# Optimization experiments

Measured on AMD Instinct MI355X. Metric: run time of the kernel, lower is better.

The kernel has to match this reference:

```python
import jax, jax.numpy as jnp
import numpy as np

B, L, D = 16, 2048, 128
NEG = -1000000.0  # fill value used by the torch module

def setup_inputs() -> dict:
    key = jax.random.key(0)
    kq, kk, kv, kl = jax.random.split(key, 4)
    Q = jax.random.normal(kq, (B, L, D), dtype=jnp.float32)
    K = jax.random.normal(kk, (B, L, D), dtype=jnp.float32)
    V = jax.random.normal(kv, (B, L, D), dtype=jnp.float32)
    valid_lens = jax.random.randint(kl, (B,), 0, L, dtype=jnp.int32)
    return {"Q": Q, "K": K, "V": V, "valid_lens": valid_lens}

def reference(Q, K, V, valid_lens):
    d = Q.shape[-1]
    scale = 1.0 / jnp.sqrt(jnp.asarray(d, Q.dtype))
    # scores: [B, Lq, Lk]
    scores = jnp.einsum("bqd,bkd->bqk", Q, K) * scale
    # mask[b, q, k] = k < valid_lens[b]  (torch code requires Lq == Lk)
    mask = jnp.arange(scores.shape[-1])[None, None, :] < valid_lens[:, None, None]
    scores = jnp.where(mask, scores, jnp.asarray(NEG, scores.dtype))
    weights = jax.nn.softmax(scores, axis=-1)
    # dropout=0.0 / eval mode -> identity
    return jnp.einsum("bqk,bkd->bqd", weights, V)
```

## Files before the change

kernel.cpp:

```cpp
#include <hip/hip_runtime.h>
#include <hip/hip_bf16.h>
#include <math.h>

#define NB 16
#define NL 2048
#define ND 128
#define QT 64
#define KT 32
#define NTILE (NL / KT)
#define NEGV -1000000.0f
#define SCL 0.08838834764831845f

typedef short bfrag __attribute__((ext_vector_type(8)));
typedef float f32x4 __attribute__((ext_vector_type(4)));
typedef short s16x4 __attribute__((ext_vector_type(4)));
typedef short s16x8 __attribute__((ext_vector_type(8)));

typedef const __attribute__((address_space(1))) void* gas_ptr;
typedef __attribute__((address_space(3))) void* las_ptr;

__device__ __forceinline__ short f2bf(float f) {
    unsigned u = __float_as_uint(f);
    unsigned r = u + 0x7FFFu + ((u >> 16) & 1u);
    return (short)(r >> 16);
}
__device__ __forceinline__ float bf2f(short h) {
    return __uint_as_float(((unsigned)(unsigned short)h) << 16);
}

__device__ __forceinline__ int kswz(int r, int c) { return (r * ND + c) ^ ((r & 7) << 3); }
__device__ __forceinline__ int vswz(int d, int k) { return (d * KT + k) ^ (((d >> 1) & 3) << 3); }
__device__ __forceinline__ int pswz(int q, int k) { return (q * KT + k) ^ (((q >> 1) & 3) << 3); }

__global__ __launch_bounds__(512) void prep_k(const float* __restrict__ Kg,
                                              short* __restrict__ KWS) {
    const int bt = blockIdx.x;
    const int g = threadIdx.x;
    const int r = g >> 4, ccd = g & 15;
    const int ccs = ccd ^ (r & 7);
    const float* src = Kg + ((size_t)((bt >> 6) * NL) + (bt & 63) * KT + r) * ND + ccs * 8;
    f32x4 a0 = *(const f32x4*)src;
    f32x4 a1 = *(const f32x4*)(src + 4);
    float vals[8] = {a0[0], a0[1], a0[2], a0[3], a1[0], a1[1], a1[2], a1[3]};
    s16x8 h, l;
    #pragma unroll
    for (int j = 0; j < 8; ++j) {
        short hb = f2bf(vals[j]);
        h[j] = hb;
        l[j] = f2bf(vals[j] - bf2f(hb));
    }
    short* dst = KWS + (size_t)bt * 2 * 4096 + g * 8;
    *(s16x8*)dst = h;
    *(s16x8*)(dst + 4096) = l;
}

__global__ __launch_bounds__(512) void prep_v(const float* __restrict__ Vg,
                                              short* __restrict__ VWS) {
    const int bt = blockIdx.x;
    const int g = threadIdx.x;
    const int ch = g >> 7, d = g & 127;
    const int chs = ch ^ ((d >> 1) & 3);
    const float* src = Vg + ((size_t)((bt >> 6) * NL) + (bt & 63) * KT + chs * 8) * ND + d;
    s16x8 h, l;
    #pragma unroll
    for (int j = 0; j < 8; ++j) {
        float f = src[(size_t)j * ND];
        short hb = f2bf(f);
        h[j] = hb;
        l[j] = f2bf(f - bf2f(hb));
    }
    short* dst = VWS + (size_t)bt * 2 * 4096 + (d * 4 + ch) * 8;
    *(s16x8*)dst = h;
    *(s16x8*)(dst + 4096) = l;
}

__global__ __launch_bounds__(256, 2) void attn_fwd(
    const float* __restrict__ Qg, const int* __restrict__ vlens,
    const short* __restrict__ KWS, const short* __restrict__ VWS,
    float* __restrict__ Og)
{
    __shared__ __align__(16) short kv[2][4][4096];
    __shared__ __align__(16) short ph[4][512], pl[4][512];

    const int tid = threadIdx.x;
    const int wv = tid >> 6, lane = tid & 63;
    const int lq = lane & 15, lg = lane >> 4;

    const int bid = blockIdx.x;
    const int xcd = bid & 7, slot = bid >> 3;
    const int b = xcd * 2 + (slot >> 5);
    const int qblk = slot & 31;
    const int q0 = qblk * QT + wv * 16;

    const int vlen = vlens[b];
    const int kmax = (vlen > 0) ? vlen : NL;
    const int ntiles = (kmax + KT - 1) / KT;

    bfrag qh[4], ql[4];
    {
        const float* qp = Qg + ((size_t)b * NL + (size_t)(q0 + lq)) * ND + lg * 8;
        #pragma unroll
        for (int s = 0; s < 4; ++s) {
            f32x4 a0 = *(const f32x4*)(qp + s * 32);
            f32x4 a1 = *(const f32x4*)(qp + s * 32 + 4);
            float vals[8] = {a0[0], a0[1], a0[2], a0[3], a1[0], a1[1], a1[2], a1[3]};
            bfrag h, l;
            #pragma unroll
            for (int j = 0; j < 8; ++j) {
                short hb = f2bf(vals[j]);
                h[j] = hb;
                l[j] = f2bf(vals[j] - bf2f(hb));
            }
            qh[s] = h; ql[s] = l;
        }
    }

    const short* kws = KWS + (size_t)b * NTILE * 2 * 4096;
    const short* vws = VWS + (size_t)b * NTILE * 2 * 4096;

    const short* src_base = (wv < 2 ? kws : vws);
    const int hl = wv & 1;

    const f32x4 zero4 = {0.f, 0.f, 0.f, 0.f};
    float m_run = -INFINITY, l_run = 0.0f;
    f32x4 oacc[8];
    #pragma unroll
    for (int i = 0; i < 8; ++i) oacc[i] = zero4;

    int cur = 0;
    {
        const short* s0 = src_base + (size_t)hl * 4096 + lane * 8;
        #pragma unroll
        for (int i = 0; i < 8; ++i)
            __builtin_amdgcn_global_load_lds((gas_ptr)(s0 + i * 512),
                                             (las_ptr)(&kv[0][wv][i * 512]), 16, 0, 0);
    }

    for (int t = 0; t < ntiles; ++t) {
        const int kt0 = t * KT;
        if (t + 1 < ntiles) {
            const short* sn = src_base + ((size_t)(t + 1) * 2 + hl) * 4096 + lane * 8;
            #pragma unroll
            for (int i = 0; i < 8; ++i)
                __builtin_amdgcn_global_load_lds((gas_ptr)(sn + i * 512),
                                                 (las_ptr)(&kv[cur ^ 1][wv][i * 512]), 16, 0, 0);
            asm volatile("s_waitcnt vmcnt(8)" ::: "memory");
        } else {
            asm volatile("s_waitcnt vmcnt(0)" ::: "memory");
        }
        __builtin_amdgcn_s_barrier();
        asm volatile("" ::: "memory");

        const short* khp = &kv[cur][0][0];
        const short* klp = &kv[cur][1][0];
        const short* vhp = &kv[cur][2][0];
        const short* vlp = &kv[cur][3][0];

        f32x4 sacc[2];
        sacc[0] = zero4; sacc[1] = zero4;
        #pragma unroll
        for (int sub = 0; sub < 2; ++sub) {
            #pragma unroll
            for (int s = 0; s < 4; ++s) {
                int ia = kswz(sub * 16 + lq, s * 32 + lg * 8);
                bfrag ah = *(const bfrag*)&khp[ia];
                bfrag al = *(const bfrag*)&klp[ia];
                sacc[sub] = __builtin_amdgcn_mfma_f32_16x16x32_bf16(ah, qh[s], sacc[sub], 0, 0, 0);
                sacc[sub] = __builtin_amdgcn_mfma_f32_16x16x32_bf16(al, qh[s], sacc[sub], 0, 0, 0);
                sacc[sub] = __builtin_amdgcn_mfma_f32_16x16x32_bf16(ah, ql[s], sacc[sub], 0, 0, 0);
            }
        }

        float sv[2][4];
        float tmax = -INFINITY;
        #pragma unroll
        for (int sub = 0; sub < 2; ++sub)
            #pragma unroll
            for (int r = 0; r < 4; ++r) {
                int kg = kt0 + sub * 16 + lg * 4 + r;
                float x = (kg < vlen) ? sacc[sub][r] * SCL : NEGV;
                sv[sub][r] = x;
                tmax = fmaxf(tmax, x);
            }
        tmax = fmaxf(tmax, __shfl_xor(tmax, 16, 64));
        tmax = fmaxf(tmax, __shfl_xor(tmax, 32, 64));
        float m_new = fmaxf(m_run, tmax);
        float corr = __expf(m_run - m_new);
        float rsum = 0.f;
        s16x4 phv[2], plv[2];
        #pragma unroll
        for (int sub = 0; sub < 2; ++sub)
            #pragma unroll
            for (int r = 0; r < 4; ++r) {
                float p = __expf(sv[sub][r] - m_new);
                rsum += p;
                short hb = f2bf(p);
                phv[sub][r] = hb;
                plv[sub][r] = f2bf(p - bf2f(hb));
            }
        rsum += __shfl_xor(rsum, 16, 64);
        rsum += __shfl_xor(rsum, 32, 64);
        l_run = l_run * corr + rsum;
        m_run = m_new;
        #pragma unroll
        for (int i = 0; i < 8; ++i) {
            oacc[i][0] *= corr; oacc[i][1] *= corr;
            oacc[i][2] *= corr; oacc[i][3] *= corr;
        }

        #pragma unroll
        for (int sub = 0; sub < 2; ++sub) {
            int ip = pswz(lq, sub * 16 + lg * 4);
            *(s16x4*)&ph[wv][ip] = phv[sub];
            *(s16x4*)&pl[wv][ip] = plv[sub];
        }
        int ipb = pswz(lq, lg * 8);
        bfrag pbh = *(const bfrag*)&ph[wv][ipb];
        bfrag pbl = *(const bfrag*)&pl[wv][ipb];

        #pragma unroll
        for (int dt = 0; dt < 8; ++dt) {
            int iv = vswz(dt * 16 + lq, lg * 8);
            bfrag vh  = *(const bfrag*)&vhp[iv];
            bfrag vlo = *(const bfrag*)&vlp[iv];
            oacc[dt] = __builtin_amdgcn_mfma_f32_16x16x32_bf16(vh,  pbh, oacc[dt], 0, 0, 0);
            oacc[dt] = __builtin_amdgcn_mfma_f32_16x16x32_bf16(vlo, pbh, oacc[dt], 0, 0, 0);
            oacc[dt] = __builtin_amdgcn_mfma_f32_16x16x32_bf16(vh,  pbl, oacc[dt], 0, 0, 0);
        }

        asm volatile("" ::: "memory");
        __builtin_amdgcn_s_barrier();
        cur ^= 1;
    }

    float inv = 1.0f / l_run;
    float* op = Og + ((size_t)b * NL + (size_t)(q0 + lq)) * ND + lg * 4;
    #pragma unroll
    for (int dt = 0; dt < 8; ++dt) {
        f32x4 o;
        o[0] = oacc[dt][0] * inv; o[1] = oacc[dt][1] * inv;
        o[2] = oacc[dt][2] * inv; o[3] = oacc[dt][3] * inv;
        *(f32x4*)(op + dt * 16) = o;
    }
}

__global__ __launch_bounds__(256, 2) void attn_fwd_fb(
    const float* __restrict__ Qg, const float* __restrict__ Kg,
    const float* __restrict__ Vg, const int* __restrict__ vlens,
    float* __restrict__ Og)
{
    __shared__ __align__(16) short kh[KT * ND], kl[KT * ND];
    __shared__ __align__(16) short vth[ND * KT], vtl[ND * KT];
    __shared__ __align__(16) short ph[4][16 * KT], pl[4][16 * KT];

    const int tid = threadIdx.x;
    const int wv = tid >> 6, lane = tid & 63;
    const int lq = lane & 15, lg = lane >> 4;
    const int bid = blockIdx.x;
    const int b = bid >> 5;
    const int qblk = bid & 31;
    const int q0 = qblk * QT + wv * 16;
    const int vlen = vlens[b];
    const int kmax = (vlen > 0) ? vlen : NL;
    const int ntiles = (kmax + KT - 1) / KT;

    bfrag qh[4], ql[4];
    {
        const float* qp = Qg + ((size_t)b * NL + (size_t)(q0 + lq)) * ND + lg * 8;
        #pragma unroll
        for (int s = 0; s < 4; ++s) {
            f32x4 a0 = *(const f32x4*)(qp + s * 32);
            f32x4 a1 = *(const f32x4*)(qp + s * 32 + 4);
            float vals[8] = {a0[0], a0[1], a0[2], a0[3], a1[0], a1[1], a1[2], a1[3]};
            bfrag h, l;
            #pragma unroll
            for (int j = 0; j < 8; ++j) {
                short hb = f2bf(vals[j]);
                h[j] = hb;
                l[j] = f2bf(vals[j] - bf2f(hb));
            }
            qh[s] = h; ql[s] = l;
        }
    }

    const f32x4 zero4 = {0.f, 0.f, 0.f, 0.f};
    float m_run = -INFINITY, l_run = 0.0f;
    f32x4 oacc[8];
    #pragma unroll
    for (int i = 0; i < 8; ++i) oacc[i] = zero4;

    const float* kbase = Kg + (size_t)b * NL * ND;
    const float* vbase = Vg + (size_t)b * NL * ND;

    for (int t = 0; t < ntiles; ++t) {
        const int kt0 = t * KT;
        __syncthreads();
        #pragma unroll
        for (int i = 0; i < 4; ++i) {
            int f = i * 256 + tid;
            int r = f >> 5, c4 = (f & 31) << 2;
            f32x4 v = *(const f32x4*)(kbase + (size_t)(kt0 + r) * ND + c4);
            s16x4 hh, ll;
            #pragma unroll
            for (int j = 0; j < 4; ++j) {
                short hb = f2bf(v[j]);
                hh[j] = hb;
                ll[j] = f2bf(v[j] - bf2f(hb));
            }
            int idx = kswz(r, c4);
            *(s16x4*)&kh[idx] = hh;
            *(s16x4*)&kl[idx] = ll;
        }
        #pragma unroll
        for (int i = 0; i < 4; ++i) {
            int tau = i * 256 + tid;
            int c = tau & 127, kq = (tau >> 7) << 2;
            s16x4 hh, ll;
            #pragma unroll
            for (int j = 0; j < 4; ++j) {
                float fv = vbase[(size_t)(kt0 + kq + j) * ND + c];
                short hb = f2bf(fv);
                hh[j] = hb;
                ll[j] = f2bf(fv - bf2f(hb));
            }
            int idx = vswz(c, kq);
            *(s16x4*)&vth[idx] = hh;
            *(s16x4*)&vtl[idx] = ll;
        }
        __syncthreads();

        f32x4 sacc[2];
        sacc[0] = zero4; sacc[1] = zero4;
        #pragma unroll
        for (int sub = 0; sub < 2; ++sub) {
            #pragma unroll
            for (int s = 0; s < 4; ++s) {
                int ia = kswz(sub * 16 + lq, s * 32 + lg * 8);
                bfrag ah = *(const bfrag*)&kh[ia];
                bfrag al = *(const bfrag*)&kl[ia];
                sacc[sub] = __builtin_amdgcn_mfma_f32_16x16x32_bf16(ah, qh[s], sacc[sub], 0, 0, 0);
                sacc[sub] = __builtin_amdgcn_mfma_f32_16x16x32_bf16(al, qh[s], sacc[sub], 0, 0, 0);
                sacc[sub] = __builtin_amdgcn_mfma_f32_16x16x32_bf16(ah, ql[s], sacc[sub], 0, 0, 0);
            }
        }

        float sv[2][4];
        float tmax = -INFINITY;
        #pragma unroll
        for (int sub = 0; sub < 2; ++sub)
            #pragma unroll
            for (int r = 0; r < 4; ++r) {
                int kg = kt0 + sub * 16 + lg * 4 + r;
                float x = (kg < vlen) ? sacc[sub][r] * SCL : NEGV;
                sv[sub][r] = x;
                tmax = fmaxf(tmax, x);
            }
        tmax = fmaxf(tmax, __shfl_xor(tmax, 16, 64));
        tmax = fmaxf(tmax, __shfl_xor(tmax, 32, 64));
        float m_new = fmaxf(m_run, tmax);
        float corr = __expf(m_run - m_new);
        float rsum = 0.f;
        s16x4 phv[2], plv[2];
        #pragma unroll
        for (int sub = 0; sub < 2; ++sub)
            #pragma unroll
            for (int r = 0; r < 4; ++r) {
                float p = __expf(sv[sub][r] - m_new);
                rsum += p;
                short hb = f2bf(p);
                phv[sub][r] = hb;
                plv[sub][r] = f2bf(p - bf2f(hb));
            }
        rsum += __shfl_xor(rsum, 16, 64);
        rsum += __shfl_xor(rsum, 32, 64);
        l_run = l_run * corr + rsum;
        m_run = m_new;
        #pragma unroll
        for (int i = 0; i < 8; ++i) {
            oacc[i][0] *= corr; oacc[i][1] *= corr;
            oacc[i][2] *= corr; oacc[i][3] *= corr;
        }

        #pragma unroll
        for (int sub = 0; sub < 2; ++sub) {
            int ip = pswz(lq, sub * 16 + lg * 4);
            *(s16x4*)&ph[wv][ip] = phv[sub];
            *(s16x4*)&pl[wv][ip] = plv[sub];
        }
        int ipb = pswz(lq, lg * 8);
        bfrag pbh = *(const bfrag*)&ph[wv][ipb];
        bfrag pbl = *(const bfrag*)&pl[wv][ipb];
        #pragma unroll
        for (int dt = 0; dt < 8; ++dt) {
            int iv = vswz(dt * 16 + lq, lg * 8);
            bfrag vh  = *(const bfrag*)&vth[iv];
            bfrag vlo = *(const bfrag*)&vtl[iv];
            oacc[dt] = __builtin_amdgcn_mfma_f32_16x16x32_bf16(vh,  pbh, oacc[dt], 0, 0, 0);
            oacc[dt] = __builtin_amdgcn_mfma_f32_16x16x32_bf16(vlo, pbh, oacc[dt], 0, 0, 0);
            oacc[dt] = __builtin_amdgcn_mfma_f32_16x16x32_bf16(vh,  pbl, oacc[dt], 0, 0, 0);
        }
    }

    float inv = 1.0f / l_run;
    float* op = Og + ((size_t)b * NL + (size_t)(q0 + lq)) * ND + lg * 4;
    #pragma unroll
    for (int dt = 0; dt < 8; ++dt) {
        f32x4 o;
        o[0] = oacc[dt][0] * inv; o[1] = oacc[dt][1] * inv;
        o[2] = oacc[dt][2] * inv; o[3] = oacc[dt][3] * inv;
        *(f32x4*)(op + dt * 16) = o;
    }
}

extern "C" void kernel_launch(void* const* d_in, const int* in_sizes, int n_in,
                              void* d_out, int out_size, void* d_ws, size_t ws_size,
                              hipStream_t stream) {
    (void)in_sizes; (void)n_in; (void)out_size;
    const float* Q = (const float*)d_in[0];
    const float* K = (const float*)d_in[1];
    const float* V = (const float*)d_in[2];
    const int* vl  = (const int*)d_in[3];
    float* O = (float*)d_out;

    const size_t tensor_bytes = (size_t)NB * NTILE * 2 * 4096 * sizeof(short);
    const size_t need = 2 * tensor_bytes;

    if (ws_size >= need) {
        short* KWS = (short*)d_ws;
        short* VWS = KWS + (size_t)NB * NTILE * 2 * 4096;
        prep_k<<<dim3(NB * NTILE), dim3(512), 0, stream>>>(K, KWS);
        prep_v<<<dim3(NB * NTILE), dim3(512), 0, stream>>>(V, VWS);
        attn_fwd<<<dim3(NB * (NL / QT)), dim3(256), 0, stream>>>(Q, vl, KWS, VWS, O);
    } else {
        attn_fwd_fb<<<dim3(NB * (NL / QT)), dim3(256), 0, stream>>>(Q, K, V, vl, O);
    }
}
```

Baseline: 193.0 us.

## Split KV range across workgroups with partial-softmax merge and skip masked prep tiles

Attention is now split along the key dimension into NS chunks per query block, with each workgroup writing partial max, sum and output to a workspace. A separate merge kernel then combines the chunks with log-sum-exp rescaling. This is meant to fix load imbalance from variable valid lengths by spreading the work of long sequences across more workgroups. The K and V prep kernels are fused into one launch that skips tiles beyond the valid length, and the split kernel stages tiles through registers with a single LDS buffer at higher occupancy. The cost is an extra launch and extra partial-result traffic through global memory.

```diff
diff --git a/kernel.cpp b/kernel.cpp
--- a/kernel.cpp
+++ b/kernel.cpp
@@ -32,46 +32,281 @@
 __device__ __forceinline__ int vswz(int d, int k) { return (d * KT + k) ^ (((d >> 1) & 3) << 3); }
 __device__ __forceinline__ int pswz(int q, int k) { return (q * KT + k) ^ (((q >> 1) & 3) << 3); }
 
-__global__ __launch_bounds__(512) void prep_k(const float* __restrict__ Kg,
-                                              short* __restrict__ KWS) {
-    const int bt = blockIdx.x;
+__global__ __launch_bounds__(512) void prep_kv(const float* __restrict__ Kg,
+                                               const float* __restrict__ Vg,
+                                               const int* __restrict__ vlens,
+                                               short* __restrict__ KWS,
+                                               short* __restrict__ VWS) {
+    const int bid = blockIdx.x;
+    const int b = bid >> 7, rem = bid & 127, t = rem >> 1, isv = rem & 1;
+    const int vlen = vlens[b];
+    const int kmax = (vlen > 0) ? vlen : NL;
+    if (t * KT >= kmax) return;
     const int g = threadIdx.x;
-    const int r = g >> 4, ccd = g & 15;
-    const int ccs = ccd ^ (r & 7);
-    const float* src = Kg + ((size_t)((bt >> 6) * NL) + (bt & 63) * KT + r) * ND + ccs * 8;
-    f32x4 a0 = *(const f32x4*)src;
-    f32x4 a1 = *(const f32x4*)(src + 4);
-    float vals[8] = {a0[0], a0[1], a0[2], a0[3], a1[0], a1[1], a1[2], a1[3]};
-    s16x8 h, l;
-    #pragma unroll
-    for (int j = 0; j < 8; ++j) {
-        short hb = f2bf(vals[j]);
-        h[j] = hb;
-        l[j] = f2bf(vals[j] - bf2f(hb));
-    }
-    short* dst = KWS + (size_t)bt * 2 * 4096 + g * 8;
-    *(s16x8*)dst = h;
-    *(s16x8*)(dst + 4096) = l;
-}
-
-__global__ __launch_bounds__(512) void prep_v(const float* __restrict__ Vg,
-                                              short* __restrict__ VWS) {
-    const int bt = blockIdx.x;
-    const int g = threadIdx.x;
-    const int ch = g >> 7, d = g & 127;
-    const int chs = ch ^ ((d >> 1) & 3);
-    const float* src = Vg + ((size_t)((bt >> 6) * NL) + (bt & 63) * KT + chs * 8) * ND + d;
-    s16x8 h, l;
-    #pragma unroll
-    for (int j = 0; j < 8; ++j) {
-        float f = src[(size_t)j * ND];
-        short hb = f2bf(f);
-        h[j] = hb;
-        l[j] = f2bf(f - bf2f(hb));
-    }
-    short* dst = VWS + (size_t)bt * 2 * 4096 + (d * 4 + ch) * 8;
-    *(s16x8*)dst = h;
-    *(s16x8*)(dst + 4096) = l;
+    const size_t bt = (size_t)(b * NTILE + t);
+    if (!isv) {
+        const int r = g >> 4, ccd = g & 15;
+        const int ccs = ccd ^ (r & 7);
+        const float* src = Kg + ((size_t)b * NL + (size_t)(t * KT + r)) * ND + ccs * 8;
+        f32x4 a0 = *(const f32x4*)src;
+        f32x4 a1 = *(const f32x4*)(src + 4);
+        float vals[8] = {a0[0], a0[1], a0[2], a0[3], a1[0], a1[1], a1[2], a1[3]};
+        s16x8 h, l;
+        #pragma unroll
+        for (int j = 0; j < 8; ++j) {
+            short hb = f2bf(vals[j]);
+            h[j] = hb;
+            l[j] = f2bf(vals[j] - bf2f(hb));
+        }
+        short* dst = KWS + bt * 8192 + g * 8;
+        *(s16x8*)dst = h;
+        *(s16x8*)(dst + 4096) = l;
+    } else {
+        const int ch = g >> 7, d = g & 127;
+        const int chs = ch ^ ((d >> 1) & 3);
+        const float* src = Vg + ((size_t)b * NL + (size_t)(t * KT + chs * 8)) * ND + d;
+        s16x8 h, l;
+        #pragma unroll
+        for (int j = 0; j < 8; ++j) {
+            float f = src[(size_t)j * ND];
+            short hb = f2bf(f);
+            h[j] = hb;
+            l[j] = f2bf(f - bf2f(hb));
+        }
+        short* dst = VWS + bt * 8192 + (d * 4 + ch) * 8;
+        *(s16x8*)dst = h;
+        *(s16x8*)(dst + 4096) = l;
+    }
+}
+
+template<int NS>
+__global__ __launch_bounds__(256, 4) void attn_split(
+    const float* __restrict__ Qg, const int* __restrict__ vlens,
+    const short* __restrict__ KWS, const short* __restrict__ VWS,
+    float* __restrict__ PWS)
+{
+    constexpr int TPH = NTILE / NS;
+    constexpr int CHUNK = NB * 32 * NS / 8;
+    __shared__ __align__(16) short kv[4][4096];
+    __shared__ __align__(16) short ph[4][512], pl[4][512];
+
+    const int tid = threadIdx.x;
+    const int wv = tid >> 6, lane = tid & 63;
+    const int lq = lane & 15, lg = lane >> 4;
+
+    const int wg = blockIdx.x;
+    const int wgid = (wg & 7) * CHUNK + (wg >> 3);
+    const int b = wgid / (32 * NS);
+    const int rem = wgid - b * (32 * NS);
+    const int qblk = rem / NS;
+    const int hh = rem - qblk * NS;
+
+    const int vlen = vlens[b];
+    const int kmax = (vlen > 0) ? vlen : NL;
+    const int nt = (kmax + KT - 1) / KT;
+    const int t0 = hh * TPH;
+    const int t1 = (nt < t0 + TPH) ? nt : (t0 + TPH);
+    if (t0 >= t1) return;
+
+    const int q0 = qblk * QT + wv * 16;
+
+    bfrag qh[4], ql[4];
+    {
+        const float* qp = Qg + ((size_t)b * NL + (size_t)(q0 + lq)) * ND + lg * 8;
+        #pragma unroll
+        for (int s = 0; s < 4; ++s) {
+            f32x4 a0 = *(const f32x4*)(qp + s * 32);
+            f32x4 a1 = *(const f32x4*)(qp + s * 32 + 4);
+            float vals[8] = {a0[0], a0[1], a0[2], a0[3], a1[0], a1[1], a1[2], a1[3]};
+            bfrag h, l;
+            #pragma unroll
+            for (int j = 0; j < 8; ++j) {
+                short hb = f2bf(vals[j]);
+                h[j] = hb;
+                l[j] = f2bf(vals[j] - bf2f(hb));
+            }
+            qh[s] = h; ql[s] = l;
+        }
+    }
+
+    const short* src = (wv < 2 ? KWS : VWS) + (size_t)b * NTILE * 8192
+                     + (size_t)(wv & 1) * 4096 + lane * 8
+                     + (size_t)t0 * 8192;
+
+    s16x8 pf[8];
+    #pragma unroll
+    for (int i = 0; i < 8; ++i)
+        pf[i] = *(const s16x8*)(src + i * 512);
+
+    const f32x4 zero4 = {0.f, 0.f, 0.f, 0.f};
+    float m_run = -INFINITY, l_run = 0.0f;
+    f32x4 oacc[8];
+    #pragma unroll
+    for (int i = 0; i < 8; ++i) oacc[i] = zero4;
+
+    for (int t = t0; t < t1; ++t) {
+        const int kt0 = t * KT;
+
+        __builtin_amdgcn_s_barrier();
+        #pragma unroll
+        for (int i = 0; i < 8; ++i)
+            *(s16x8*)&kv[wv][i * 512 + lane * 8] = pf[i];
+        asm volatile("s_waitcnt lgkmcnt(0)" ::: "memory");
+        __builtin_amdgcn_sched_barrier(0);
+        __builtin_amdgcn_s_barrier();
+
+        src += 8192;
+        if (t + 1 < t1) {
+            #pragma unroll
+            for (int i = 0; i < 8; ++i)
+                pf[i] = *(const s16x8*)(src + i * 512);
+        }
+
+        f32x4 sacc[2];
+        sacc[0] = zero4; sacc[1] = zero4;
+        #pragma unroll
+        for (int sub = 0; sub < 2; ++sub) {
+            #pragma unroll
+            for (int s = 0; s < 4; ++s) {
+                int ia = kswz(sub * 16 + lq, s * 32 + lg * 8);
+                bfrag ah = *(const bfrag*)&kv[0][ia];
+                bfrag al = *(const bfrag*)&kv[1][ia];
+                sacc[sub] = __builtin_amdgcn_mfma_f32_16x16x32_bf16(ah, qh[s], sacc[sub], 0, 0, 0);
+                sacc[sub] = __builtin_amdgcn_mfma_f32_16x16x32_bf16(al, qh[s], sacc[sub], 0, 0, 0);
+                sacc[sub] = __builtin_amdgcn_mfma_f32_16x16x32_bf16(ah, ql[s], sacc[sub], 0, 0, 0);
+            }
+        }
+
+        float sv[2][4];
+        float tmax = -INFINITY;
+        #pragma unroll
+        for (int sub = 0; sub < 2; ++sub)
+            #pragma unroll
+            for (int r = 0; r < 4; ++r) {
+                int kg = kt0 + sub * 16 + lg * 4 + r;
+                float x = (kg < vlen) ? sacc[sub][r] * SCL : NEGV;
+                sv[sub][r] = x;
+                tmax = fmaxf(tmax, x);
+            }
+        tmax = fmaxf(tmax, __shfl_xor(tmax, 16, 64));
+        tmax = fmaxf(tmax, __shfl_xor(tmax, 32, 64));
+        if (!__all(tmax <= m_run + 8.0f)) {
+            float m_new = fmaxf(m_run, tmax);
+            float corr = __expf(m_run - m_new);
+            l_run *= corr;
+            #pragma unroll
+            for (int i = 0; i < 8; ++i) {
+                oacc[i][0] *= corr; oacc[i][1] *= corr;
+                oacc[i][2] *= corr; oacc[i][3] *= corr;
+            }
+            m_run = m_new;
+        }
+        float rsum = 0.f;
+        s16x4 phv[2], plv[2];
+        #pragma unroll
+        for (int sub = 0; sub < 2; ++sub)
+            #pragma unroll
+            for (int r = 0; r < 4; ++r) {
+                float p = __expf(sv[sub][r] - m_run);
+                rsum += p;
+                short hb = f2bf(p);
+                phv[sub][r] = hb;
+                plv[sub][r] = f2bf(p - bf2f(hb));
+            }
+        rsum += __shfl_xor(rsum, 16, 64);
+        rsum += __shfl_xor(rsum, 32, 64);
+        l_run += rsum;
+
+        #pragma unroll
+        for (int sub = 0; sub < 2; ++sub) {
+            int ip = pswz(lq, sub * 16 + lg * 4);
+            *(s16x4*)&ph[wv][ip] = phv[sub];
+            *(s16x4*)&pl[wv][ip] = plv[sub];
+        }
+        int ipb = pswz(lq, lg * 8);
+        bfrag pbh = *(const bfrag*)&ph[wv][ipb];
+        bfrag pbl = *(const bfrag*)&pl[wv][ipb];
+
+        #pragma unroll
+        for (int dt = 0; dt < 8; ++dt) {
+            int iv = vswz(dt * 16 + lq, lg * 8);
+            bfrag vh  = *(const bfrag*)&kv[2][iv];
+            bfrag vlo = *(const bfrag*)&kv[3][iv];
+            oacc[dt] = __builtin_amdgcn_mfma_f32_16x16x32_bf16(vh,  pbh, oacc[dt], 0, 0, 0);
+            oacc[dt] = __builtin_amdgcn_mfma_f32_16x16x32_bf16(vlo, pbh, oacc[dt], 0, 0, 0);
+            oacc[dt] = __builtin_amdgcn_mfma_f32_16x16x32_bf16(vh,  pbl, oacc[dt], 0, 0, 0);
+        }
+    }
+
+    const size_t unit = (size_t)(b * 32 + qblk) * NS + hh;
+    float* pw = PWS + unit * (128 + 64 * 128);
+    if (lg == 0) {
+        pw[wv * 16 + lq] = m_run;
+        pw[64 + wv * 16 + lq] = l_run;
+    }
+    float* po = pw + 128 + (size_t)(wv * 16 + lq) * 128 + lg * 4;
+    #pragma unroll
+    for (int dt = 0; dt < 8; ++dt)
+        *(f32x4*)(po + dt * 16) = oacc[dt];
+}
+
+template<int NS>
+__global__ __launch_bounds__(256) void merge_part(
+    const int* __restrict__ vlens, const float* __restrict__ PWS,
+    float* __restrict__ Og)
+{
+    constexpr int TPH = NTILE / NS;
+    const int bid = blockIdx.x;
+    const int b = bid >> 5, qblk = bid & 31;
+    const int vlen = vlens[b];
+    const int kmax = (vlen > 0) ? vlen : NL;
+    const int nt = (kmax + KT - 1) / KT;
+    int nh = (nt + TPH - 1) / TPH;
+    if (nh > NS) nh = NS;
+
+    const int tid = threadIdx.x;
+    const int q = tid >> 2;
+    const int d0 = (tid & 3) * 32;
+
+    const float* base = PWS + (size_t)((b * 32 + qblk) * NS) * (128 + 64 * 128);
+
+    float mh[NS], lh[NS];
+    float M = -INFINITY;
+    #pragma unroll
+    for (int h = 0; h < NS; ++h) {
+        if (h < nh) {
+            const float* pw = base + (size_t)h * (128 + 64 * 128);
+            mh[h] = pw[q];
+            lh[h] = pw[64 + q];
+        } else { mh[h] = -INFINITY; lh[h] = 0.f; }
+        M = fmaxf(M, mh[h]);
+    }
+    float w[NS];
+    float L = 0.f;
+    #pragma unroll
+    for (int h = 0; h < NS; ++h) {
+        w[h] = __expf(mh[h] - M);
+        L += lh[h] * w[h];
+    }
+    const float inv = 1.0f / L;
+
+    float* out = Og + ((size_t)b * NL + (size_t)(qblk * 64 + q)) * ND + d0;
+    #pragma unroll
+    for (int c = 0; c < 8; ++c) {
+        f32x4 acc = {0.f, 0.f, 0.f, 0.f};
+        #pragma unroll
+        for (int h = 0; h < NS; ++h) {
+            if (h < nh) {
+                const float* po = base + (size_t)h * (128 + 64 * 128) + 128
+                                + (size_t)q * 128 + d0 + c * 4;
+                f32x4 v = *(const f32x4*)po;
+                acc[0] += v[0] * w[h]; acc[1] += v[1] * w[h];
+                acc[2] += v[2] * w[h]; acc[3] += v[3] * w[h];
+            }
+        }
+        acc[0] *= inv; acc[1] *= inv; acc[2] *= inv; acc[3] *= inv;
+        *(f32x4*)(out + c * 4) = acc;
+    }
 }
 
 __global__ __launch_bounds__(256, 2) void attn_fwd(
@@ -115,9 +350,8 @@
         }
     }
 
-    const short* kws = KWS + (size_t)b * NTILE * 2 * 4096;
-    const short* vws = VWS + (size_t)b * NTILE * 2 * 4096;
-
+    const short* kws = KWS + (size_t)b * NTILE * 8192;
+    const short* vws = VWS + (size_t)b * NTILE * 8192;
     const short* src_base = (wv < 2 ? kws : vws);
     const int hl = wv & 1;
 
@@ -151,11 +385,6 @@
         __builtin_amdgcn_s_barrier();
         asm volatile("" ::: "memory");
 
-        const short* khp = &kv[cur][0][0];
-        const short* klp = &kv[cur][1][0];
-        const short* vhp = &kv[cur][2][0];
-        const short* vlp = &kv[cur][3][0];
-
         f32x4 sacc[2];
         sacc[0] = zero4; sacc[1] = zero4;
         #pragma unroll
@@ -163,8 +392,8 @@
             #pragma unroll
             for (int s = 0; s < 4; ++s) {
                 int ia = kswz(sub * 16 + lq, s * 32 + lg * 8);
-                bfrag ah = *(const bfrag*)&khp[ia];
-                bfrag al = *(const bfrag*)&klp[ia];
+                bfrag ah = *(const bfrag*)&kv[cur][0][ia];
+                bfrag al = *(const bfrag*)&kv[cur][1][ia];
                 sacc[sub] = __builtin_amdgcn_mfma_f32_16x16x32_bf16(ah, qh[s], sacc[sub], 0, 0, 0);
                 sacc[sub] = __builtin_amdgcn_mfma_f32_16x16x32_bf16(al, qh[s], sacc[sub], 0, 0, 0);
                 sacc[sub] = __builtin_amdgcn_mfma_f32_16x16x32_bf16(ah, ql[s], sacc[sub], 0, 0, 0);
@@ -221,8 +450,8 @@
         #pragma unroll
         for (int dt = 0; dt < 8; ++dt) {
             int iv = vswz(dt * 16 + lq, lg * 8);
-            bfrag vh  = *(const bfrag*)&vhp[iv];
-            bfrag vlo = *(const bfrag*)&vlp[iv];
+            bfrag vh  = *(const bfrag*)&kv[cur][2][iv];
+            bfrag vlo = *(const bfrag*)&kv[cur][3][iv];
             oacc[dt] = __builtin_amdgcn_mfma_f32_16x16x32_bf16(vh,  pbh, oacc[dt], 0, 0, 0);
             oacc[dt] = __builtin_amdgcn_mfma_f32_16x16x32_bf16(vlo, pbh, oacc[dt], 0, 0, 0);
             oacc[dt] = __builtin_amdgcn_mfma_f32_16x16x32_bf16(vh,  pbl, oacc[dt], 0, 0, 0);
@@ -422,14 +651,26 @@
     const int* vl  = (const int*)d_in[3];
     float* O = (float*)d_out;
 
-    const size_t tensor_bytes = (size_t)NB * NTILE * 2 * 4096 * sizeof(short);
-    const size_t need = 2 * tensor_bytes;
-
-    if (ws_size >= need) {
-        short* KWS = (short*)d_ws;
-        short* VWS = KWS + (size_t)NB * NTILE * 2 * 4096;
-        prep_k<<<dim3(NB * NTILE), dim3(512), 0, stream>>>(K, KWS);
-        prep_v<<<dim3(NB * NTILE), dim3(512), 0, stream>>>(V, VWS);
+    const size_t tensor_shorts = (size_t)NB * NTILE * 8192;
+    const size_t kv_bytes = 2 * tensor_shorts * sizeof(short);
+    const size_t unit_floats = 128 + 64 * 128;
+    const size_t pws4 = (size_t)NB * 32 * 4 * unit_floats * 4;
+    const size_t pws2 = (size_t)NB * 32 * 2 * unit_floats * 4;
+
+    short* KWS = (short*)d_ws;
+    short* VWS = KWS + tensor_shorts;
+    float* PWS = (float*)((char*)d_ws + kv_bytes);
+
+    if (ws_size >= kv_bytes + pws4) {
+        prep_kv<<<dim3(NB * NTILE * 2), dim3(512), 0, stream>>>(K, V, vl, KWS, VWS);
+        attn_split<4><<<dim3(NB * 32 * 4), dim3(256), 0, stream>>>(Q, vl, KWS, VWS, PWS);
+        merge_part<4><<<dim3(NB * 32), dim3(256), 0, stream>>>(vl, PWS, O);
+    } else if (ws_size >= kv_bytes + pws2) {
+        prep_kv<<<dim3(NB * NTILE * 2), dim3(512), 0, stream>>>(K, V, vl, KWS, VWS);
+        attn_split<2><<<dim3(NB * 32 * 2), dim3(256), 0, stream>>>(Q, vl, KWS, VWS, PWS);
+        merge_part<2><<<dim3(NB * 32), dim3(256), 0, stream>>>(vl, PWS, O);
+    } else if (ws_size >= kv_bytes) {
+        prep_kv<<<dim3(NB * NTILE * 2), dim3(512), 0, stream>>>(K, V, vl, KWS, VWS);
         attn_fwd<<<dim3(NB * (NL / QT)), dim3(256), 0, stream>>>(Q, vl, KWS, VWS, O);
     } else {
         attn_fwd_fb<<<dim3(NB * (NL / QT)), dim3(256), 0, stream>>>(Q, K, V, vl, O);
```

Measured after the change: 314.2 us. 1.63x slower.
